# Performance work log

Hardware: AMD Instinct MI355X
Metric: run time of the kernel (lower is better)

Reference implementation:

```python
import jax, jax.numpy as jnp
import numpy as np
from jax import lax

B, N, C = 2, 4096, 8
MAX_DET = 100
SCORE_THR = 0.01
NMS_THR = 0.5
NEG = -1e30  # sentinel for masked scores


def setup_inputs() -> dict:
    key = jax.random.key(0)
    k1, k2, k3, k4, k5 = jax.random.split(key, 5)
    # valid xyxy boxes: centers in [0,512), extents in [2,66)
    ctr = jax.random.uniform(k1, (B, N, 2), dtype=jnp.float32) * 512.0
    wh = jax.random.uniform(k2, (B, N, 2), dtype=jnp.float32) * 64.0 + 2.0
    boxes = jnp.concatenate([ctr - wh / 2, ctr + wh / 2], axis=-1)  # [B,N,4]
    classification = jax.random.uniform(k3, (B, N, C), dtype=jnp.float32)
    rotation = jax.random.normal(k4, (B, N, 3), dtype=jnp.float32)
    translation = jax.random.normal(k5, (B, N, 3), dtype=jnp.float32)
    return {"boxes": boxes, "classification": classification,
            "rotation": rotation, "translation": translation}


def _pairwise_iou(b):
    # b: [N,4] xyxy, torchvision convention (no +1)
    x1, y1, x2, y2 = b[:, 0], b[:, 1], b[:, 2], b[:, 3]
    area = (x2 - x1) * (y2 - y1)
    ix1 = jnp.maximum(x1[:, None], x1[None, :])
    iy1 = jnp.maximum(y1[:, None], y1[None, :])
    ix2 = jnp.minimum(x2[:, None], x2[None, :])
    iy2 = jnp.minimum(y2[:, None], y2[None, :])
    inter = jnp.clip(ix2 - ix1, 0.0) * jnp.clip(iy2 - iy1, 0.0)
    union = area[:, None] + area[None, :] - inter
    return inter / jnp.maximum(union, 1e-9)


def _nms_keep(boxes, scores, valid):
    # greedy NMS matching torchvision.ops.nms on the `valid` subset.
    order = jnp.argsort(-jnp.where(valid, scores, NEG))  # score-descending
    iou = _pairwise_iou(boxes[order])  # [N,N]
    idx = jnp.arange(N)
    keep0 = valid[order]

    def body(i, keep):
        sup = keep[i] & (iou[i] > NMS_THR) & (idx > i)
        return keep & ~sup

    keep_sorted = lax.fori_loop(0, N, body, keep0)
    return jnp.zeros(N, bool).at[order].set(keep_sorted)


def _filter_image(boxes, cls, rot, trans):
    # boxes [N,4], cls [N,C], rot [N,3], trans [N,3]
    def per_class(scores):
        valid = scores > SCORE_THR
        keep = _nms_keep(boxes, scores, valid)
        return jnp.where(keep, scores, NEG)

    masked = jax.vmap(per_class, in_axes=1)(cls)  # [C,N]
    topv, topi = lax.top_k(masked.reshape(-1), MAX_DET)
    labels = topi // N
    anchors = topi % N
    ok = topv > NEG / 2
    okc = ok[:, None]
    boxes_o = jnp.where(okc, boxes[anchors], -1.0)
    scores_o = jnp.where(ok, topv, -1.0)
    labels_o = jnp.where(ok, labels, -1)
    rot_o = jnp.where(okc, rot[anchors], -1.0)
    trans_o = jnp.where(okc, trans[anchors], -1.0)
    return boxes_o, scores_o, labels_o, rot_o, trans_o


def reference(boxes, classification, rotation, translation):
    return jax.vmap(_filter_image)(boxes, classification, rotation, translation)
```

## Files before the change

### kernel.cpp

```cpp
#include <hip/hip_runtime.h>
#include <hip/hip_bf16.h>
#include <stdint.h>

#define B_ 2
#define N_ 4096
#define C_ 8
#define MAXDET 100
#define SCORE_THR 0.01f
#define NMS_THR 0.5f
#define NEGV -1e30f

typedef unsigned long long u64;

__device__ __forceinline__ unsigned mono_key(float f) {
    unsigned u = __float_as_uint(f);
    return (u & 0x80000000u) ? ~u : (u | 0x80000000u);
}
__device__ __forceinline__ float mono_dec(unsigned m) {
    return (m & 0x80000000u) ? __uint_as_float(m ^ 0x80000000u)
                             : __uint_as_float(~m);
}
__device__ __forceinline__ bool iou_gt_half(float inter, float uni) {
    return (inter + inter - uni) > uni * 0x1p-25f;
}
__device__ __forceinline__ void wave_fence() {
    asm volatile("s_waitcnt lgkmcnt(0)" ::: "memory");
}

__global__ __launch_bounds__(512) void sortA_kernel(
    const float* __restrict__ cls,
    u64* __restrict__ keys)
{
    __shared__ u64 k[1024];
    const int q = blockIdx.x;
    const int bc = blockIdx.y;
    const int b = bc >> 3, c = bc & 7;
    const int tid = threadIdx.x;
    const bool desc = ((q & 1) == 0);

    for (int li = tid; li < 1024; li += 512) {
        int i = q * 1024 + li;
        float s = cls[((size_t)b * N_ + i) * C_ + c];
        float f = (s > SCORE_THR) ? s : NEGV;
        k[li] = ((u64)mono_key(f) << 32) | (unsigned)(~i);
    }
    __syncthreads();

    for (int size = 2; size <= 1024; size <<= 1) {
        for (int stride = size >> 1; stride > 0; stride >>= 1) {
            int t = tid;
            int pos = 2 * t - (t & (stride - 1));
            int par = pos + stride;
            bool d = ((pos & size) == 0) ? desc : !desc;
            u64 a = k[pos], bb = k[par];
            if ((a < bb) == d) { k[pos] = bb; k[par] = a; }
            __syncthreads();
        }
    }

    for (int li = tid; li < 1024; li += 512)
        keys[(size_t)bc * N_ + q * 1024 + li] = k[li];
}

__global__ __launch_bounds__(512) void fused_kernel(
    const u64* __restrict__ keys,
    const float* __restrict__ boxes,
    u64* __restrict__ cand)
{
    __shared__ u64 m[4096];
    __shared__ float4 sb192[192];
    __shared__ float  sa192[192];
    __shared__ u64 cm[576];
    __shared__ float4 sbx[64];
    __shared__ u64 shJ[64];
    __shared__ int s_fin;

    const int bc = blockIdx.x;
    const int b = bc >> 3, cls = bc & 7;
    const int tid = threadIdx.x;
    const int lane = tid & 63;
    const int wave = tid >> 6;
    const size_t kbase = (size_t)bc * N_;
    const float4* boxes4 = (const float4*)boxes;

    {
        int i = tid;
        int q = i >> 8;
        int off = q * 1024 + ((q & 1) ? 768 : 0) + (i & 255);
        m[i] = keys[kbase + off];
        i = tid + 512; q = i >> 8;
        off = q * 1024 + ((q & 1) ? 768 : 0) + (i & 255);
        m[i] = keys[kbase + off];
    }
    __syncthreads();

    for (int size = 512; size <= 1024; size <<= 1) {
        for (int stride = size >> 1; stride > 0; stride >>= 1) {
            int pos = 2 * tid - (tid & (stride - 1));
            int par = pos + stride;
            bool d = ((pos & size) == 0);
            u64 a = m[pos], bb = m[par];
            if ((a < bb) == d) { m[pos] = bb; m[par] = a; }
            __syncthreads();
        }
    }

    if (tid < 192) {
        int orig = (int)(~(unsigned)m[tid]);
        float4 bx = boxes4[(size_t)b * N_ + orig];
        sb192[tid] = bx;
        sa192[tid] = (bx.z - bx.x) * (bx.w - bx.y);
    }
    __syncthreads();

    for (int qq = tid; qq < 576; qq += 512) {
        int r = qq / 3, w = qq - 3 * r;
        int chunk = r >> 6;
        u64 bits = 0ull;
        if (w >= chunk) {
            float4 bi = sb192[r];
            float aarea = sa192[r];
            #pragma unroll 8
            for (int t = 0; t < 64; t++) {
                float4 bj = sb192[w * 64 + t];
                float barea = sa192[w * 64 + t];
                float ix1 = fmaxf(bi.x, bj.x);
                float iy1 = fmaxf(bi.y, bj.y);
                float ix2 = fminf(bi.z, bj.z);
                float iy2 = fminf(bi.w, bj.w);
                float inter = fmaxf(ix2 - ix1, 0.0f) * fmaxf(iy2 - iy1, 0.0f);
                float uni = fmaxf(aarea + barea - inter, 1e-9f);
                if (iou_gt_half(inter, uni)) bits |= (1ull << t);
            }
            if (w == chunk) bits &= ~((2ull << (r & 63)) - 1ull);
        }
        cm[qq] = bits;
    }
    __syncthreads();

    if (wave == 0) {
        u64 remv = 0ull;
        int cc = 0;
        bool fin = false;
        for (int c = 0; c < 3; c++) {
            int p = c * 64 + lane;
            u64 key = m[p];
            float sc = mono_dec((unsigned)(key >> 32));
            u64 validb = __ballot(sc > -1e29f);
            if (validb == 0ull) { fin = true; break; }

            u64 curw = __shfl(remv, c, 64);
            u64 kept = 0ull;
            for (int t = 0; t < 64; t++) {
                u64 iv = cm[(c * 64 + t) * 3 + c];
                u64 bit = 1ull << t;
                if (!(curw & bit) && (validb & bit)) { kept |= bit; curw |= iv; }
            }

            if ((kept >> lane) & 1ull) {
                int rank = cc + __popcll(kept & ((1ull << lane) - 1ull));
                if (rank < 128) {
                    int orig = (int)(~(unsigned)key);
                    unsigned flat = (unsigned)(cls * N_ + orig);
                    cand[bc * 128 + rank] =
                        ((u64)mono_key(sc) << 32) | (unsigned)(~flat);
                }
            }
            cc += __popcll(kept);
            if (cc >= 128) { fin = true; break; }

            if (lane < 3) {
                u64 acc = 0ull;
                for (int t = 0; t < 64; t++)
                    if ((kept >> t) & 1ull) acc |= cm[(c * 64 + t) * 3 + lane];
                remv |= acc;
            }
        }
        if (fin) {
            int filled = cc < 128 ? cc : 128;
            for (int s = lane; s < 128; s += 64)
                if (s >= filled) cand[bc * 128 + s] = 0ull;
        }
        if (lane == 0) s_fin = fin ? 1 : 0;
    }
    __syncthreads();
    if (s_fin) return;

    for (int i = tid; i < 4096; i += 512) m[i] = keys[kbase + i];
    __syncthreads();
    for (int size = 2048; size <= 4096; size <<= 1) {
        for (int stride = size >> 1; stride > 0; stride >>= 1) {
            for (int t = tid; t < 2048; t += 512) {
                int pos = 2 * t - (t & (stride - 1));
                int par = pos + stride;
                bool d = ((pos & size) == 0);
                u64 a = m[pos], bb = m[par];
                if ((a < bb) == d) { m[pos] = bb; m[par] = a; }
            }
            __syncthreads();
        }
    }
    if (wave != 0) return;

    {
        u64 remv = 0ull;
        int cc = 0;
        for (int c = 0; c < 64; c++) {
            int p = c * 64 + lane;
            u64 key = m[p];
            float sc = mono_dec((unsigned)(key >> 32));
            u64 validb = __ballot(sc > -1e29f);
            if (validb == 0ull) break;

            int orig = (int)(~(unsigned)key);
            float4 bl = boxes4[(size_t)b * N_ + orig];
            sbx[lane] = bl;
            wave_fence();
            float al = (bl.z - bl.x) * (bl.w - bl.y);

            u64 intra = 0ull;
            for (int t = 0; t < 64; t++) {
                float4 bj = sbx[t];
                float ab = (bj.z - bj.x) * (bj.w - bj.y);
                float ix1 = fmaxf(bl.x, bj.x);
                float iy1 = fmaxf(bl.y, bj.y);
                float ix2 = fminf(bl.z, bj.z);
                float iy2 = fminf(bl.w, bj.w);
                float inter = fmaxf(ix2 - ix1, 0.0f) * fmaxf(iy2 - iy1, 0.0f);
                float uni = fmaxf(al + ab - inter, 1e-9f);
                if (t > lane && iou_gt_half(inter, uni)) intra |= (1ull << t);
            }
            shJ[lane] = intra;
            wave_fence();

            u64 curw = __shfl(remv, c, 64);
            u64 kept = 0ull;
            for (int t = 0; t < 64; t++) {
                u64 iv = shJ[t];
                u64 bit = 1ull << t;
                if (!(curw & bit) && (validb & bit)) { kept |= bit; curw |= iv; }
            }

            if ((kept >> lane) & 1ull) {
                int rank = cc + __popcll(kept & ((1ull << lane) - 1ull));
                if (rank < 128) {
                    unsigned flat = (unsigned)(cls * N_ + orig);
                    cand[bc * 128 + rank] =
                        ((u64)mono_key(sc) << 32) | (unsigned)(~flat);
                }
            }
            cc += __popcll(kept);
            if (cc >= 128) break;

            if (lane > c) {
                u64 accw = 0ull;
                for (int u = 0; u < 64; u++) {
                    int pj = lane * 64 + u;
                    int oj = (int)(~(unsigned)m[pj]);
                    float4 bj = boxes4[(size_t)b * N_ + oj];
                    float ab = (bj.z - bj.x) * (bj.w - bj.y);
                    bool sup = false;
                    for (int tt = 0; tt < 64; tt++) {
                        if (!((kept >> tt) & 1ull)) continue;
                        float4 br = sbx[tt];
                        float ar = (br.z - br.x) * (br.w - br.y);
                        float ix1 = fmaxf(br.x, bj.x);
                        float iy1 = fmaxf(br.y, bj.y);
                        float ix2 = fminf(br.z, bj.z);
                        float iy2 = fminf(br.w, bj.w);
                        float inter = fmaxf(ix2 - ix1, 0.0f) * fmaxf(iy2 - iy1, 0.0f);
                        float uni = fmaxf(ar + ab - inter, 1e-9f);
                        if (iou_gt_half(inter, uni)) { sup = true; break; }
                    }
                    if (sup) accw |= (1ull << u);
                }
                remv |= accw;
            }
            wave_fence();
        }
        int filled = cc < 128 ? cc : 128;
        for (int s = lane; s < 128; s += 64)
            if (s >= filled) cand[bc * 128 + s] = 0ull;
    }
}

__global__ __launch_bounds__(1024) void merge_kernel(
    const u64* __restrict__ cand,
    const float* __restrict__ boxes,
    const float* __restrict__ rot,
    const float* __restrict__ trans,
    float* __restrict__ out)
{
    __shared__ u64 sk[1024];
    const int b = blockIdx.x;
    const int tid = threadIdx.x;
    const int c = tid >> 7, s = tid & 127;

    int src = (c & 1) ? (c * 128 + (127 - s)) : tid;
    sk[tid] = cand[(size_t)b * 1024 + src];

    for (int size = 256; size <= 1024; size <<= 1) {
        for (int stride = size >> 1; stride > 0; stride >>= 1) {
            __syncthreads();
            int partner = tid ^ stride;
            if (partner > tid) {
                bool desc = ((tid & size) == 0);
                u64 a = sk[tid], bb = sk[partner];
                if ((a < bb) == desc) { sk[tid] = bb; sk[partner] = a; }
            }
        }
    }
    __syncthreads();

    if (tid < MAXDET) {
        u64 key = sk[tid];
        float score = mono_dec((unsigned)(key >> 32));
        bool ok = score > (NEGV * 0.5f);
        unsigned flat = (~(unsigned)key) & 32767u;
        int cc = flat >> 12;
        int n = flat & (N_ - 1);

        float* obox = out;
        float* oscr = out + 800;
        float* olab = out + 1000;
        float* orot = out + 1200;
        float* otrn = out + 1800;

        #pragma unroll
        for (int d = 0; d < 4; d++)
            obox[b * 400 + tid * 4 + d] =
                ok ? boxes[((size_t)b * N_ + n) * 4 + d] : -1.0f;
        oscr[b * MAXDET + tid] = ok ? score : -1.0f;
        olab[b * MAXDET + tid] = ok ? (float)cc : -1.0f;
        #pragma unroll
        for (int d = 0; d < 3; d++) {
            orot[b * 300 + tid * 3 + d] =
                ok ? rot[((size_t)b * N_ + n) * 3 + d] : -1.0f;
            otrn[b * 300 + tid * 3 + d] =
                ok ? trans[((size_t)b * N_ + n) * 3 + d] : -1.0f;
        }
    }
}

extern "C" void kernel_launch(void* const* d_in, const int* in_sizes, int n_in,
                              void* d_out, int out_size, void* d_ws, size_t ws_size,
                              hipStream_t stream) {
    const float* boxes = (const float*)d_in[0];
    const float* cls   = (const float*)d_in[1];
    const float* rot   = (const float*)d_in[2];
    const float* trans = (const float*)d_in[3];
    float* out = (float*)d_out;

    char* w = (char*)d_ws;
    u64* keys = (u64*)w;   w += (size_t)B_ * C_ * N_ * sizeof(u64);
    u64* cand = (u64*)w;   w += (size_t)B_ * C_ * 128 * sizeof(u64);

    sortA_kernel<<<dim3(4, B_ * C_), 512, 0, stream>>>(cls, keys);
    fused_kernel<<<B_ * C_, 512, 0, stream>>>(keys, boxes, cand);
    merge_kernel<<<B_, 1024, 0, stream>>>(cand, boxes, rot, trans, out);
}
```

Measured before the change: 99.58 us.

## Fuse initial per-chunk bitonic sort into main NMS kernel, drop global key buffer

Moves the chunked bitonic sort of class scores from a separate 64-block kernel into the per-class kernel, building keys directly in shared memory. This removes a kernel launch and the global write/read of the key array, and the later full sort reuses the in-LDS keys. The trade-off is that the first sort now runs on only 16 blocks, with each thread doing four compare-swaps per step.

After: 122.9 us. 23.5% more time.

```diff
diff --git a/kernel.cpp b/kernel.cpp
--- a/kernel.cpp
+++ b/kernel.cpp
@@ -27,47 +27,13 @@
     asm volatile("s_waitcnt lgkmcnt(0)" ::: "memory");
 }
 
-__global__ __launch_bounds__(512) void sortA_kernel(
-    const float* __restrict__ cls,
-    u64* __restrict__ keys)
-{
-    __shared__ u64 k[1024];
-    const int q = blockIdx.x;
-    const int bc = blockIdx.y;
-    const int b = bc >> 3, c = bc & 7;
-    const int tid = threadIdx.x;
-    const bool desc = ((q & 1) == 0);
-
-    for (int li = tid; li < 1024; li += 512) {
-        int i = q * 1024 + li;
-        float s = cls[((size_t)b * N_ + i) * C_ + c];
-        float f = (s > SCORE_THR) ? s : NEGV;
-        k[li] = ((u64)mono_key(f) << 32) | (unsigned)(~i);
-    }
-    __syncthreads();
-
-    for (int size = 2; size <= 1024; size <<= 1) {
-        for (int stride = size >> 1; stride > 0; stride >>= 1) {
-            int t = tid;
-            int pos = 2 * t - (t & (stride - 1));
-            int par = pos + stride;
-            bool d = ((pos & size) == 0) ? desc : !desc;
-            u64 a = k[pos], bb = k[par];
-            if ((a < bb) == d) { k[pos] = bb; k[par] = a; }
-            __syncthreads();
-        }
-    }
-
-    for (int li = tid; li < 1024; li += 512)
-        keys[(size_t)bc * N_ + q * 1024 + li] = k[li];
-}
-
-__global__ __launch_bounds__(512) void fused_kernel(
-    const u64* __restrict__ keys,
+__global__ __launch_bounds__(512) void mega_kernel(
+    const float* __restrict__ cls_in,
     const float* __restrict__ boxes,
     u64* __restrict__ cand)
 {
     __shared__ u64 m[4096];
+    __shared__ u64 m2[1024];
     __shared__ float4 sb192[192];
     __shared__ float  sa192[192];
     __shared__ u64 cm[576];
@@ -80,33 +46,47 @@
     const int tid = threadIdx.x;
     const int lane = tid & 63;
     const int wave = tid >> 6;
-    const size_t kbase = (size_t)bc * N_;
     const float4* boxes4 = (const float4*)boxes;
 
-    {
-        int i = tid;
+    for (int i = tid; i < 4096; i += 512) {
+        float s = cls_in[((size_t)b * N_ + i) * C_ + cls];
+        float f = (s > SCORE_THR) ? s : NEGV;
+        m[i] = ((u64)mono_key(f) << 32) | (unsigned)(~i);
+    }
+    __syncthreads();
+
+    for (int size = 2; size <= 1024; size <<= 1) {
+        for (int stride = size >> 1; stride > 0; stride >>= 1) {
+            for (int t = tid; t < 2048; t += 512) {
+                int pos = 2 * t - (t & (stride - 1));
+                int par = pos + stride;
+                bool d = ((pos & size) == 0);
+                u64 a = m[pos], bb = m[par];
+                if ((a < bb) == d) { m[pos] = bb; m[par] = a; }
+            }
+            __syncthreads();
+        }
+    }
+
+    for (int i = tid; i < 1024; i += 512) {
         int q = i >> 8;
         int off = q * 1024 + ((q & 1) ? 768 : 0) + (i & 255);
-        m[i] = keys[kbase + off];
-        i = tid + 512; q = i >> 8;
-        off = q * 1024 + ((q & 1) ? 768 : 0) + (i & 255);
-        m[i] = keys[kbase + off];
-    }
-    __syncthreads();
-
+        m2[i] = m[off];
+    }
+    __syncthreads();
     for (int size = 512; size <= 1024; size <<= 1) {
         for (int stride = size >> 1; stride > 0; stride >>= 1) {
             int pos = 2 * tid - (tid & (stride - 1));
             int par = pos + stride;
             bool d = ((pos & size) == 0);
-            u64 a = m[pos], bb = m[par];
-            if ((a < bb) == d) { m[pos] = bb; m[par] = a; }
+            u64 a = m2[pos], bb = m2[par];
+            if ((a < bb) == d) { m2[pos] = bb; m2[par] = a; }
             __syncthreads();
         }
     }
 
     if (tid < 192) {
-        int orig = (int)(~(unsigned)m[tid]);
+        int orig = (int)(~(unsigned)m2[tid]);
         float4 bx = boxes4[(size_t)b * N_ + orig];
         sb192[tid] = bx;
         sa192[tid] = (bx.z - bx.x) * (bx.w - bx.y);
@@ -144,7 +124,7 @@
         bool fin = false;
         for (int c = 0; c < 3; c++) {
             int p = c * 64 + lane;
-            u64 key = m[p];
+            u64 key = m2[p];
             float sc = mono_dec((unsigned)(key >> 32));
             u64 validb = __ballot(sc > -1e29f);
             if (validb == 0ull) { fin = true; break; }
@@ -186,8 +166,6 @@
     __syncthreads();
     if (s_fin) return;
 
-    for (int i = tid; i < 4096; i += 512) m[i] = keys[kbase + i];
-    __syncthreads();
     for (int size = 2048; size <= 4096; size <<= 1) {
         for (int stride = size >> 1; stride > 0; stride >>= 1) {
             for (int t = tid; t < 2048; t += 512) {
@@ -352,10 +330,8 @@
     float* out = (float*)d_out;
 
     char* w = (char*)d_ws;
-    u64* keys = (u64*)w;   w += (size_t)B_ * C_ * N_ * sizeof(u64);
     u64* cand = (u64*)w;   w += (size_t)B_ * C_ * 128 * sizeof(u64);
 
-    sortA_kernel<<<dim3(4, B_ * C_), 512, 0, stream>>>(cls, keys);
-    fused_kernel<<<B_ * C_, 512, 0, stream>>>(keys, boxes, cand);
+    mega_kernel<<<B_ * C_, 512, 0, stream>>>(cls, boxes, cand);
     merge_kernel<<<B_, 1024, 0, stream>>>(cand, boxes, rot, trans, out);
 }
```

## Fuse merge into NMS kernel via last-block atomic ticket; pad sort LDS

Applied to the files above, without the earlier changes.

The separate merge kernel is removed. Each per-class block now takes an atomic ticket per image, and the last block for that image runs the final bitonic merge and output gather, which saves one kernel launch and its dependency gap. A counter memset is added to the stream, and the merge now runs with 512 threads instead of 1024. Separately, the sortA shared-memory indices are padded to cut LDS bank conflicts in the bitonic sort. The added risk is the fence and ticket pattern, plus the extra memset.

Result: slower. 103.1 us (+3.6%).

```diff
diff --git a/kernel.cpp b/kernel.cpp
--- a/kernel.cpp
+++ b/kernel.cpp
@@ -12,6 +12,8 @@
 
 typedef unsigned long long u64;
 
+#define SW(i) ((i) + ((i) >> 4))
+
 __device__ __forceinline__ unsigned mono_key(float f) {
     unsigned u = __float_as_uint(f);
     return (u & 0x80000000u) ? ~u : (u | 0x80000000u);
@@ -31,7 +33,7 @@
     const float* __restrict__ cls,
     u64* __restrict__ keys)
 {
-    __shared__ u64 k[1024];
+    __shared__ u64 k[1024 + 64];
     const int q = blockIdx.x;
     const int bc = blockIdx.y;
     const int b = bc >> 3, c = bc & 7;
@@ -42,7 +44,7 @@
         int i = q * 1024 + li;
         float s = cls[((size_t)b * N_ + i) * C_ + c];
         float f = (s > SCORE_THR) ? s : NEGV;
-        k[li] = ((u64)mono_key(f) << 32) | (unsigned)(~i);
+        k[SW(li)] = ((u64)mono_key(f) << 32) | (unsigned)(~i);
     }
     __syncthreads();
 
@@ -52,20 +54,24 @@
             int pos = 2 * t - (t & (stride - 1));
             int par = pos + stride;
             bool d = ((pos & size) == 0) ? desc : !desc;
-            u64 a = k[pos], bb = k[par];
-            if ((a < bb) == d) { k[pos] = bb; k[par] = a; }
+            u64 a = k[SW(pos)], bb = k[SW(par)];
+            if ((a < bb) == d) { k[SW(pos)] = bb; k[SW(par)] = a; }
             __syncthreads();
         }
     }
 
     for (int li = tid; li < 1024; li += 512)
-        keys[(size_t)bc * N_ + q * 1024 + li] = k[li];
+        keys[(size_t)bc * N_ + q * 1024 + li] = k[SW(li)];
 }
 
 __global__ __launch_bounds__(512) void fused_kernel(
     const u64* __restrict__ keys,
     const float* __restrict__ boxes,
-    u64* __restrict__ cand)
+    const float* __restrict__ rot,
+    const float* __restrict__ trans,
+    u64* __restrict__ cand,
+    int* __restrict__ cnt,
+    float* __restrict__ out)
 {
     __shared__ u64 m[4096];
     __shared__ float4 sb192[192];
@@ -74,6 +80,7 @@
     __shared__ float4 sbx[64];
     __shared__ u64 shJ[64];
     __shared__ int s_fin;
+    __shared__ int s_tick;
 
     const int bc = blockIdx.x;
     const int b = bc >> 3, cls = bc & 7;
@@ -184,140 +191,135 @@
         if (lane == 0) s_fin = fin ? 1 : 0;
     }
     __syncthreads();
-    if (s_fin) return;
-
-    for (int i = tid; i < 4096; i += 512) m[i] = keys[kbase + i];
-    __syncthreads();
-    for (int size = 2048; size <= 4096; size <<= 1) {
-        for (int stride = size >> 1; stride > 0; stride >>= 1) {
-            for (int t = tid; t < 2048; t += 512) {
-                int pos = 2 * t - (t & (stride - 1));
-                int par = pos + stride;
-                bool d = ((pos & size) == 0);
-                u64 a = m[pos], bb = m[par];
-                if ((a < bb) == d) { m[pos] = bb; m[par] = a; }
-            }
-            __syncthreads();
-        }
-    }
-    if (wave != 0) return;
-
-    {
-        u64 remv = 0ull;
-        int cc = 0;
-        for (int c = 0; c < 64; c++) {
-            int p = c * 64 + lane;
-            u64 key = m[p];
-            float sc = mono_dec((unsigned)(key >> 32));
-            u64 validb = __ballot(sc > -1e29f);
-            if (validb == 0ull) break;
-
-            int orig = (int)(~(unsigned)key);
-            float4 bl = boxes4[(size_t)b * N_ + orig];
-            sbx[lane] = bl;
-            wave_fence();
-            float al = (bl.z - bl.x) * (bl.w - bl.y);
-
-            u64 intra = 0ull;
-            for (int t = 0; t < 64; t++) {
-                float4 bj = sbx[t];
-                float ab = (bj.z - bj.x) * (bj.w - bj.y);
-                float ix1 = fmaxf(bl.x, bj.x);
-                float iy1 = fmaxf(bl.y, bj.y);
-                float ix2 = fminf(bl.z, bj.z);
-                float iy2 = fminf(bl.w, bj.w);
-                float inter = fmaxf(ix2 - ix1, 0.0f) * fmaxf(iy2 - iy1, 0.0f);
-                float uni = fmaxf(al + ab - inter, 1e-9f);
-                if (t > lane && iou_gt_half(inter, uni)) intra |= (1ull << t);
-            }
-            shJ[lane] = intra;
-            wave_fence();
-
-            u64 curw = __shfl(remv, c, 64);
-            u64 kept = 0ull;
-            for (int t = 0; t < 64; t++) {
-                u64 iv = shJ[t];
-                u64 bit = 1ull << t;
-                if (!(curw & bit) && (validb & bit)) { kept |= bit; curw |= iv; }
-            }
-
-            if ((kept >> lane) & 1ull) {
-                int rank = cc + __popcll(kept & ((1ull << lane) - 1ull));
-                if (rank < 128) {
-                    unsigned flat = (unsigned)(cls * N_ + orig);
-                    cand[bc * 128 + rank] =
-                        ((u64)mono_key(sc) << 32) | (unsigned)(~flat);
-                }
-            }
-            cc += __popcll(kept);
-            if (cc >= 128) break;
-
-            if (lane > c) {
-                u64 accw = 0ull;
-                for (int u = 0; u < 64; u++) {
-                    int pj = lane * 64 + u;
-                    int oj = (int)(~(unsigned)m[pj]);
-                    float4 bj = boxes4[(size_t)b * N_ + oj];
+
+    if (!s_fin) {
+        for (int i = tid; i < 4096; i += 512) m[i] = keys[kbase + i];
+        __syncthreads();
+        for (int size = 2048; size <= 4096; size <<= 1) {
+            for (int stride = size >> 1; stride > 0; stride >>= 1) {
+                for (int t = tid; t < 2048; t += 512) {
+                    int pos = 2 * t - (t & (stride - 1));
+                    int par = pos + stride;
+                    bool d = ((pos & size) == 0);
+                    u64 a = m[pos], bb = m[par];
+                    if ((a < bb) == d) { m[pos] = bb; m[par] = a; }
+                }
+                __syncthreads();
+            }
+        }
+        if (wave == 0) {
+            u64 remv = 0ull;
+            int cc = 0;
+            for (int c = 0; c < 64; c++) {
+                int p = c * 64 + lane;
+                u64 key = m[p];
+                float sc = mono_dec((unsigned)(key >> 32));
+                u64 validb = __ballot(sc > -1e29f);
+                if (validb == 0ull) break;
+
+                int orig = (int)(~(unsigned)key);
+                float4 bl = boxes4[(size_t)b * N_ + orig];
+                sbx[lane] = bl;
+                wave_fence();
+                float al = (bl.z - bl.x) * (bl.w - bl.y);
+
+                u64 intra = 0ull;
+                for (int t = 0; t < 64; t++) {
+                    float4 bj = sbx[t];
                     float ab = (bj.z - bj.x) * (bj.w - bj.y);
-                    bool sup = false;
-                    for (int tt = 0; tt < 64; tt++) {
-                        if (!((kept >> tt) & 1ull)) continue;
-                        float4 br = sbx[tt];
-                        float ar = (br.z - br.x) * (br.w - br.y);
-                        float ix1 = fmaxf(br.x, bj.x);
-                        float iy1 = fmaxf(br.y, bj.y);
-                        float ix2 = fminf(br.z, bj.z);
-                        float iy2 = fminf(br.w, bj.w);
-                        float inter = fmaxf(ix2 - ix1, 0.0f) * fmaxf(iy2 - iy1, 0.0f);
-                        float uni = fmaxf(ar + ab - inter, 1e-9f);
-                        if (iou_gt_half(inter, uni)) { sup = true; break; }
+                    float ix1 = fmaxf(bl.x, bj.x);
+                    float iy1 = fmaxf(bl.y, bj.y);
+                    float ix2 = fminf(bl.z, bj.z);
+                    float iy2 = fminf(bl.w, bj.w);
+                    float inter = fmaxf(ix2 - ix1, 0.0f) * fmaxf(iy2 - iy1, 0.0f);
+                    float uni = fmaxf(al + ab - inter, 1e-9f);
+                    if (t > lane && iou_gt_half(inter, uni)) intra |= (1ull << t);
+                }
+                shJ[lane] = intra;
+                wave_fence();
+
+                u64 curw = __shfl(remv, c, 64);
+                u64 kept = 0ull;
+                for (int t = 0; t < 64; t++) {
+                    u64 iv = shJ[t];
+                    u64 bit = 1ull << t;
+                    if (!(curw & bit) && (validb & bit)) { kept |= bit; curw |= iv; }
+                }
+
+                if ((kept >> lane) & 1ull) {
+                    int rank = cc + __popcll(kept & ((1ull << lane) - 1ull));
+                    if (rank < 128) {
+                        unsigned flat = (unsigned)(cls * N_ + orig);
+                        cand[bc * 128 + rank] =
+                            ((u64)mono_key(sc) << 32) | (unsigned)(~flat);
                     }
-                    if (sup) accw |= (1ull << u);
-                }
-                remv |= accw;
-            }
-            wave_fence();
-        }
-        int filled = cc < 128 ? cc : 128;
-        for (int s = lane; s < 128; s += 64)
-            if (s >= filled) cand[bc * 128 + s] = 0ull;
-    }
-}
-
-__global__ __launch_bounds__(1024) void merge_kernel(
-    const u64* __restrict__ cand,
-    const float* __restrict__ boxes,
-    const float* __restrict__ rot,
-    const float* __restrict__ trans,
-    float* __restrict__ out)
-{
-    __shared__ u64 sk[1024];
-    const int b = blockIdx.x;
-    const int tid = threadIdx.x;
-    const int c = tid >> 7, s = tid & 127;
-
-    int src = (c & 1) ? (c * 128 + (127 - s)) : tid;
-    sk[tid] = cand[(size_t)b * 1024 + src];
+                }
+                cc += __popcll(kept);
+                if (cc >= 128) break;
+
+                if (lane > c) {
+                    u64 accw = 0ull;
+                    for (int u = 0; u < 64; u++) {
+                        int pj = lane * 64 + u;
+                        int oj = (int)(~(unsigned)m[pj]);
+                        float4 bj = boxes4[(size_t)b * N_ + oj];
+                        float ab = (bj.z - bj.x) * (bj.w - bj.y);
+                        bool sup = false;
+                        for (int tt = 0; tt < 64; tt++) {
+                            if (!((kept >> tt) & 1ull)) continue;
+                            float4 br = sbx[tt];
+                            float ar = (br.z - br.x) * (br.w - br.y);
+                            float ix1 = fmaxf(br.x, bj.x);
+                            float iy1 = fmaxf(br.y, bj.y);
+                            float ix2 = fminf(br.z, bj.z);
+                            float iy2 = fminf(br.w, bj.w);
+                            float inter = fmaxf(ix2 - ix1, 0.0f) * fmaxf(iy2 - iy1, 0.0f);
+                            float uni = fmaxf(ar + ab - inter, 1e-9f);
+                            if (iou_gt_half(inter, uni)) { sup = true; break; }
+                        }
+                        if (sup) accw |= (1ull << u);
+                    }
+                    remv |= accw;
+                }
+                wave_fence();
+            }
+            int filled = cc < 128 ? cc : 128;
+            for (int s = lane; s < 128; s += 64)
+                if (s >= filled) cand[bc * 128 + s] = 0ull;
+        }
+    }
+
+    __threadfence();
+    __syncthreads();
+    if (tid == 0) s_tick = atomicAdd(&cnt[b], 1);
+    __syncthreads();
+    if (s_tick != C_ - 1) return;
+    __threadfence();
+
+    for (int i = tid; i < 1024; i += 512) {
+        int c2 = i >> 7, s2 = i & 127;
+        int src = (c2 & 1) ? (c2 * 128 + (127 - s2)) : i;
+        m[i] = cand[(size_t)b * 1024 + src];
+    }
+    __syncthreads();
 
     for (int size = 256; size <= 1024; size <<= 1) {
         for (int stride = size >> 1; stride > 0; stride >>= 1) {
+            int pos = 2 * tid - (tid & (stride - 1));
+            int par = pos + stride;
+            bool d = ((pos & size) == 0);
+            u64 a = m[pos], bb = m[par];
+            if ((a < bb) == d) { m[pos] = bb; m[par] = a; }
             __syncthreads();
-            int partner = tid ^ stride;
-            if (partner > tid) {
-                bool desc = ((tid & size) == 0);
-                u64 a = sk[tid], bb = sk[partner];
-                if ((a < bb) == desc) { sk[tid] = bb; sk[partner] = a; }
-            }
-        }
-    }
-    __syncthreads();
+        }
+    }
 
     if (tid < MAXDET) {
-        u64 key = sk[tid];
+        u64 key = m[tid];
         float score = mono_dec((unsigned)(key >> 32));
         bool ok = score > (NEGV * 0.5f);
         unsigned flat = (~(unsigned)key) & 32767u;
-        int cc = flat >> 12;
+        int cc2 = flat >> 12;
         int n = flat & (N_ - 1);
 
         float* obox = out;
@@ -331,7 +333,7 @@
             obox[b * 400 + tid * 4 + d] =
                 ok ? boxes[((size_t)b * N_ + n) * 4 + d] : -1.0f;
         oscr[b * MAXDET + tid] = ok ? score : -1.0f;
-        olab[b * MAXDET + tid] = ok ? (float)cc : -1.0f;
+        olab[b * MAXDET + tid] = ok ? (float)cc2 : -1.0f;
         #pragma unroll
         for (int d = 0; d < 3; d++) {
             orot[b * 300 + tid * 3 + d] =
@@ -354,8 +356,10 @@
     char* w = (char*)d_ws;
     u64* keys = (u64*)w;   w += (size_t)B_ * C_ * N_ * sizeof(u64);
     u64* cand = (u64*)w;   w += (size_t)B_ * C_ * 128 * sizeof(u64);
-
+    int* cnt  = (int*)w;   w += B_ * sizeof(int);
+
+    hipMemsetAsync(cnt, 0, B_ * sizeof(int), stream);
     sortA_kernel<<<dim3(4, B_ * C_), 512, 0, stream>>>(cls, keys);
-    fused_kernel<<<B_ * C_, 512, 0, stream>>>(keys, boxes, cand);
-    merge_kernel<<<B_, 1024, 0, stream>>>(cand, boxes, rot, trans, out);
-}
+    fused_kernel<<<B_ * C_, 512, 0, stream>>>(keys, boxes, rot, trans,
+                                              cand, cnt, out);
+}
```
